# Performance work log

Hardware: AMD Instinct MI355X
Metric: run time of the kernel (lower is better)

Reference implementation:

```python
import jax, jax.numpy as jnp
import numpy as np


def _mk_mat(rows):
    # rows: list of 3 lists of (B,) arrays, written as matrix rows.
    # torch code stacks rows at dim=2, which transposes: replicate that.
    M = jnp.stack([jnp.stack(r, axis=1) for r in rows], axis=1)  # (B,3,3) written-rows
    return jnp.swapaxes(M, 1, 2)  # matches torch.stack(..., dim=2)


def _compose_mats(affine, scale, translate, shear):
    B = affine.shape[0]
    one = jnp.ones((B,), affine.dtype)
    zero = jnp.zeros((B,), affine.dtype)
    cx, sx = jnp.cos(affine[:, 0]), jnp.sin(affine[:, 0])
    cy, sy = jnp.cos(affine[:, 1]), jnp.sin(affine[:, 1])
    cz, sz = jnp.cos(affine[:, 2]), jnp.sin(affine[:, 2])
    rot_x = _mk_mat([[one, zero, zero], [zero, cx, -sx], [zero, sx, cx]])
    rot_y = _mk_mat([[cy, zero, sy], [zero, one, zero], [-sy, zero, cy]])
    rot_z = _mk_mat([[cz, -sz, zero], [sz, cz, zero], [zero, zero, one]])
    scale_m = _mk_mat([[scale[:, 0], zero, zero], [zero, scale[:, 1], zero], [zero, zero, scale[:, 2]]])
    t = jnp.tan(shear)
    shear_m = _mk_mat([[one, t[:, 0], t[:, 1]], [t[:, 2], one, t[:, 3]], [t[:, 4], t[:, 5], one]])
    trans = translate[:, :, None]  # (B,3,1)
    mat3 = shear_m @ (scale_m @ (rot_z @ (rot_y @ rot_x)))  # (B,3,3)
    inv3 = jnp.linalg.inv(mat3)
    mat = jnp.concatenate([mat3, trans], axis=-1)  # (B,3,4)
    inv_trans = jnp.matmul(-inv3, trans)
    inv_mat = jnp.concatenate([inv3, inv_trans], axis=-1)
    return mat, inv_mat


def _affine_grid(mat, D, H, W):
    # torch affine_grid, align_corners=False: coord_i = (2*i+1)/n - 1
    dt = mat.dtype
    xs = (jnp.arange(W, dtype=dt) + 0.5) * (2.0 / W) - 1.0
    ys = (jnp.arange(H, dtype=dt) + 0.5) * (2.0 / H) - 1.0
    zs = (jnp.arange(D, dtype=dt) + 0.5) * (2.0 / D) - 1.0
    zz, yy, xx = jnp.meshgrid(zs, ys, xs, indexing='ij')
    coords = jnp.stack([xx, yy, zz], axis=-1)  # (D,H,W,3) in (x,y,z) order
    grid = jnp.einsum('bkj,dhwj->bdhwk', mat[:, :, :3], coords) + mat[:, None, None, None, :, 3]
    return grid  # (B,D,H,W,3)


def _grid_sample_trilinear(src, grid):
    # torch grid_sample, mode='bilinear' (trilinear in 3D), padding zeros, align_corners=False
    B, C, D, H, W = src.shape
    ix = (grid[..., 0] + 1.0) * (W * 0.5) - 0.5
    iy = (grid[..., 1] + 1.0) * (H * 0.5) - 0.5
    iz = (grid[..., 2] + 1.0) * (D * 0.5) - 0.5
    fx, fy, fz = jnp.floor(ix), jnp.floor(iy), jnp.floor(iz)
    wx, wy, wz = ix - fx, iy - fy, iz - fz  # fractional weights
    x0, y0, z0 = fx.astype(jnp.int32), fy.astype(jnp.int32), fz.astype(jnp.int32)
    x1, y1, z1 = x0 + 1, y0 + 1, z0 + 1
    N = D * H * W
    src_flat = src.reshape(B, C, N)

    def gather(z, y, x):
        valid = (x >= 0) & (x < W) & (y >= 0) & (y < H) & (z >= 0) & (z < D)
        xi = jnp.clip(x, 0, W - 1)
        yi = jnp.clip(y, 0, H - 1)
        zi = jnp.clip(z, 0, D - 1)
        idx = ((zi * H + yi) * W + xi).reshape(B, 1, N)
        v = jnp.take_along_axis(src_flat, jnp.broadcast_to(idx, (B, C, N)), axis=2)
        return v * valid.reshape(B, 1, N).astype(src.dtype)

    def w(a):
        return a.reshape(B, 1, N)

    out = (gather(z0, y0, x0) * w((1 - wz) * (1 - wy) * (1 - wx))
           + gather(z0, y0, x1) * w((1 - wz) * (1 - wy) * wx)
           + gather(z0, y1, x0) * w((1 - wz) * wy * (1 - wx))
           + gather(z0, y1, x1) * w((1 - wz) * wy * wx)
           + gather(z1, y0, x0) * w(wz * (1 - wy) * (1 - wx))
           + gather(z1, y0, x1) * w(wz * (1 - wy) * wx)
           + gather(z1, y1, x0) * w(wz * wy * (1 - wx))
           + gather(z1, y1, x1) * w(wz * wy * wx))
    return out.reshape(B, C, D, H, W)


def setup_inputs() -> dict:
    key = jax.random.key(0)
    k1, k2, k3, k4, k5 = jax.random.split(key, 5)
    B, C, D, H, W = 2, 1, 192, 192, 192
    src = jax.random.normal(k1, (B, C, D, H, W), dtype=jnp.float32)
    affine = jax.random.uniform(k2, (B, 3), dtype=jnp.float32)
    scale = jax.random.uniform(k3, (B, 3), dtype=jnp.float32)
    translate = jax.random.uniform(k4, (B, 3), dtype=jnp.float32)
    shear = jax.random.uniform(k5, (B, 6), dtype=jnp.float32)
    return {"src": src, "affine": affine, "scale": scale, "translate": translate, "shear": shear}


def reference(src, affine, scale, translate, shear):
    B, C, D, H, W = src.shape
    mat, inv_mat = _compose_mats(affine, scale, translate, shear)
    grid = _affine_grid(mat, D, H, W)
    warped = _grid_sample_trilinear(src, grid)
    return warped, mat, inv_mat
```

## Files before the change

### kernel.cpp

```cpp
#include <hip/hip_runtime.h>
#include <math.h>

#define Bv 2
#define Dv 192
#define Hv 192
#define Wv 192
#define Nv (Dv*Hv*Wv)
#define NOUT (Bv*Nv)

#define TLZ 8
#define SWID 32
#define CAPF 16000

typedef float v2f __attribute__((ext_vector_type(2)));

__device__ __forceinline__ void mm3(const float a[3][3], const float b[3][3], float c[3][3]) {
#pragma unroll
    for (int i = 0; i < 3; ++i)
#pragma unroll
        for (int j = 0; j < 3; ++j)
            c[i][j] = a[i][0]*b[0][j] + a[i][1]*b[1][j] + a[i][2]*b[2][j];
}

__global__ void compose_mats_kernel(const float* __restrict__ affine,
                                    const float* __restrict__ scale,
                                    const float* __restrict__ translate,
                                    const float* __restrict__ shear,
                                    float* __restrict__ mats_out) {
    int b = threadIdx.x;
    if (b >= Bv) return;

    float ax = affine[b*3+0], ay = affine[b*3+1], az = affine[b*3+2];
    float cx = cosf(ax), sx = sinf(ax);
    float cy = cosf(ay), sy = sinf(ay);
    float cz = cosf(az), sz = sinf(az);

    float rx[3][3] = {{1.f,0.f,0.f},{0.f,cx,sx},{0.f,-sx,cx}};
    float ry[3][3] = {{cy,0.f,-sy},{0.f,1.f,0.f},{sy,0.f,cy}};
    float rz[3][3] = {{cz,sz,0.f},{-sz,cz,0.f},{0.f,0.f,1.f}};

    float t0 = tanf(shear[b*6+0]), t1 = tanf(shear[b*6+1]), t2 = tanf(shear[b*6+2]);
    float t3 = tanf(shear[b*6+3]), t4 = tanf(shear[b*6+4]), t5 = tanf(shear[b*6+5]);
    float sh[3][3] = {{1.f,t2,t4},{t0,1.f,t5},{t1,t3,1.f}};

    float s0 = scale[b*3+0], s1 = scale[b*3+1], s2 = scale[b*3+2];

    float m1[3][3], m2[3][3], m3s[3][3], mat3[3][3];
    mm3(ry, rx, m1);
    mm3(rz, m1, m2);
#pragma unroll
    for (int j = 0; j < 3; ++j) { m3s[0][j] = s0*m2[0][j]; m3s[1][j] = s1*m2[1][j]; m3s[2][j] = s2*m2[2][j]; }
    mm3(sh, m3s, mat3);

    float tr0 = translate[b*3+0], tr1 = translate[b*3+1], tr2 = translate[b*3+2];

    float a00 = mat3[0][0], a01 = mat3[0][1], a02 = mat3[0][2];
    float a10 = mat3[1][0], a11 = mat3[1][1], a12 = mat3[1][2];
    float a20 = mat3[2][0], a21 = mat3[2][1], a22 = mat3[2][2];
    float c00 =  (a11*a22 - a12*a21);
    float c01 = -(a10*a22 - a12*a20);
    float c02 =  (a10*a21 - a11*a20);
    float det = a00*c00 + a01*c01 + a02*c02;
    float rdet = 1.0f / det;
    float inv3[3][3];
    inv3[0][0] = c00*rdet;
    inv3[0][1] = (a02*a21 - a01*a22)*rdet;
    inv3[0][2] = (a01*a12 - a02*a11)*rdet;
    inv3[1][0] = c01*rdet;
    inv3[1][1] = (a00*a22 - a02*a20)*rdet;
    inv3[1][2] = (a02*a10 - a00*a12)*rdet;
    inv3[2][0] = c02*rdet;
    inv3[2][1] = (a01*a20 - a00*a21)*rdet;
    inv3[2][2] = (a00*a11 - a01*a10)*rdet;

    float* mo = mats_out + b*12;
#pragma unroll
    for (int i = 0; i < 3; ++i) {
        mo[i*4+0] = mat3[i][0]; mo[i*4+1] = mat3[i][1]; mo[i*4+2] = mat3[i][2];
    }
    mo[0*4+3] = tr0; mo[1*4+3] = tr1; mo[2*4+3] = tr2;

    float* io = mats_out + 24 + b*12;
#pragma unroll
    for (int i = 0; i < 3; ++i) {
        io[i*4+0] = inv3[i][0]; io[i*4+1] = inv3[i][1]; io[i*4+2] = inv3[i][2];
        io[i*4+3] = -(inv3[i][0]*tr0 + inv3[i][1]*tr1 + inv3[i][2]*tr2);
    }
}

__device__ __forceinline__ float2 ld2(const float* p) {
    float2 r;
    __builtin_memcpy(&r, p, 8);
    return r;
}

__device__ __forceinline__ void gld_lds4(const float* g, float* l) {
    __builtin_amdgcn_global_load_lds(
        (const __attribute__((address_space(1))) unsigned int*)g,
        (__attribute__((address_space(3))) unsigned int*)l, 4, 0, 0);
}

__global__ __launch_bounds__(512) void warp_kernel(const float* __restrict__ src,
                                                   const float* __restrict__ mats,
                                                   float* __restrict__ out) {
    __shared__ float stage[CAPF];

    int t   = threadIdx.x;
    int lx  = t & 15;
    int ly  = (t >> 4) & 15;
    int lzt = t >> 8;

    int W0 = blockIdx.x * 16;
    int H0 = blockIdx.y * 16;
    int zt = blockIdx.z;
    int b  = zt / (Dv/TLZ);
    int Z0 = (zt % (Dv/TLZ)) * TLZ;

    const float* M = mats + b*12;
    float m00 = M[0], m01 = M[1],  m02 = M[2],  m03 = M[3];
    float m10 = M[4], m11 = M[5],  m12 = M[6],  m13 = M[7];
    float m20 = M[8], m21 = M[9],  m22 = M[10], m23 = M[11];

    float Cx = 96.0f*(m03 - m00 - m01 - m02) + 95.5f;
    float Cy = 96.0f*(m13 - m10 - m11 - m12) + 95.5f;
    float Cz = 96.0f*(m23 - m20 - m21 - m22) + 95.5f;

    const float* sb = src + (size_t)b * Nv;

    float bcx = W0 + 8.0f, bcy = H0 + 8.0f, bcz = Z0 + 4.0f;
    float cxv = fmaf(m00, bcx, fmaf(m01, bcy, fmaf(m02, bcz, Cx)));
    float cyv = fmaf(m10, bcx, fmaf(m11, bcy, fmaf(m12, bcz, Cy)));
    float czv = fmaf(m20, bcx, fmaf(m21, bcy, fmaf(m22, bcz, Cz)));
    float hxv = 7.5f*fabsf(m00) + 7.5f*fabsf(m01) + 3.5f*fabsf(m02);
    float hyv = 7.5f*fabsf(m10) + 7.5f*fabsf(m11) + 3.5f*fabsf(m12);
    float hzv = 7.5f*fabsf(m20) + 7.5f*fabsf(m21) + 3.5f*fabsf(m22);

    int xlo = (int)floorf(cxv - hxv), xhi1 = (int)floorf(cxv + hxv) + 1;
    int ylo = (int)floorf(cyv - hyv), yhi1 = (int)floorf(cyv + hyv) + 1;
    int zlo = (int)floorf(czv - hzv), zhi1 = (int)floorf(czv + hzv) + 1;

    int bx0 = min(max(xlo, 0), Wv - SWID);
    int ey_s = min(yhi1 - ylo + 1, 64);
    int nP  = (ey_s + 1) >> 1;
    int PST = 68*nP + 4;
    int ez_need = zhi1 - zlo + 1;
    int ez_s = min(ez_need, CAPF / PST);
    int by0 = min(max(ylo, 0), Hv - 2*nP);
    int bz0 = min(max(zlo + ((ez_need - ez_s) >> 1), 0), Dv - max(ez_s, 0));

    bool uok = (xhi1 >= 0) & (xlo < Wv) & (yhi1 >= 0) & (ylo < Hv) &
               (zhi1 >= 0) & (zlo < Dv) & (ez_s >= 2) & (ey_s >= 2);
    if (!uok) ez_s = 0;

    int w = W0 + lx, h = H0 + ly;
    float fw = w + 0.5f, fh = h + 0.5f;
    float fz0 = Z0 + lzt*4 + 0.5f;

    int lane = t & 63;
    int wvu  = __builtin_amdgcn_readfirstlane(t >> 6);
    int lrow = lane >> 5;
    int col  = lane & 31;
    int srcb = (bz0*Hv + by0)*Wv + bx0 + lrow*Wv + col;
    for (int dz = wvu; dz < ez_s; dz += 8) {
        int sp = srcb + dz*(Hv*Wv);
        int lb = dz*PST;
        for (int j = 0; j < nP; ++j) {
            gld_lds4(sb + sp, &stage[lb + j*68]);
            sp += 2*Wv;
        }
    }

    float ixb = fmaf(m00, fw, fmaf(m01, fh, fmaf(m02, fz0, Cx)));
    float iyb = fmaf(m10, fw, fmaf(m11, fh, fmaf(m12, fz0, Cy)));
    float izb = fmaf(m20, fw, fmaf(m21, fh, fmaf(m22, fz0, Cz)));

    asm volatile("s_waitcnt vmcnt(0)" ::: "memory");
    __syncthreads();

    auto direct_sample = [&](float ix, float iy, float iz) -> float {
        float flx = floorf(ix), fly = floorf(iy), flz = floorf(iz);
        float wx = ix - flx, wy = iy - fly, wz = iz - flz;
        int x0 = (int)flx, y0 = (int)fly, z0 = (int)flz;
        bool all_in = ((unsigned)x0 < (unsigned)(Wv-1)) &
                      ((unsigned)y0 < (unsigned)(Hv-1)) &
                      ((unsigned)z0 < (unsigned)(Dv-1));
        if (all_in) {
            const float* p = sb + ((z0*Hv + y0)*Wv + x0);
            const float* q = p + Hv*Wv;
            float2 v00 = ld2(p);
            float2 v01 = ld2(p + Wv);
            float2 v10 = ld2(q);
            float2 v11 = ld2(q + Wv);
            float c00 = fmaf(wx, v00.y - v00.x, v00.x);
            float c01 = fmaf(wx, v01.y - v01.x, v01.x);
            float c10 = fmaf(wx, v10.y - v10.x, v10.x);
            float c11 = fmaf(wx, v11.y - v11.x, v11.x);
            float c0  = fmaf(wy, c01 - c00, c00);
            float c1  = fmaf(wy, c11 - c10, c10);
            return fmaf(wz, c1 - c0, c0);
        }
        int x1 = x0 + 1, y1 = y0 + 1, z1 = z0 + 1;
        bool all_out = (x1 < 0) | (x0 >= Wv) | (y1 < 0) | (y0 >= Hv) | (z1 < 0) | (z0 >= Dv);
        if (all_out) return 0.0f;
        auto gather = [&](int zz, int yy, int xx) -> float {
            bool valid = ((unsigned)xx < (unsigned)Wv) &
                         ((unsigned)yy < (unsigned)Hv) &
                         ((unsigned)zz < (unsigned)Dv);
            int xi = min(max(xx, 0), Wv-1);
            int yi = min(max(yy, 0), Hv-1);
            int zi = min(max(zz, 0), Dv-1);
            float val = sb[(zi*Hv + yi)*Wv + xi];
            return valid ? val : 0.0f;
        };
        float owx = 1.0f - wx, owy = 1.0f - wy, owz = 1.0f - wz;
        float a;
        a  = gather(z0, y0, x0) * (owz*owy*owx);
        a += gather(z0, y0, x1) * (owz*owy*wx);
        a += gather(z0, y1, x0) * (owz*wy*owx);
        a += gather(z0, y1, x1) * (owz*wy*wx);
        a += gather(z1, y0, x0) * (wz*owy*owx);
        a += gather(z1, y0, x1) * (wz*owy*wx);
        a += gather(z1, y1, x0) * (wz*wy*owx);
        a += gather(z1, y1, x1) * (wz*wy*wx);
        return a;
    };

    float accs[4];

#pragma unroll
    for (int zp = 0; zp < 2; ++zp) {
        float zA = (float)(2*zp), zB = (float)(2*zp + 1);
        float ixA = fmaf(m02, zA, ixb), ixB = fmaf(m02, zB, ixb);
        float iyA = fmaf(m12, zA, iyb), iyB = fmaf(m12, zB, iyb);
        float izA = fmaf(m22, zA, izb), izB = fmaf(m22, zB, izb);

        float fxA = floorf(ixA), fxB = floorf(ixB);
        float fyA = floorf(iyA), fyB = floorf(iyB);
        float fzA = floorf(izA), fzB = floorf(izB);

        int dxA = (int)fxA - bx0, dxB = (int)fxB - bx0;
        int dyA = (int)fyA - by0, dyB = (int)fyB - by0;
        int dzA = (int)fzA - bz0, dzB = (int)fzB - bz0;

        bool okA = ((unsigned)dxA <= (unsigned)(SWID-2)) &
                   ((unsigned)dyA <= (unsigned)(ey_s-2)) &
                   ((unsigned)dzA <= (unsigned)(ez_s-2));
        bool okB = ((unsigned)dxB <= (unsigned)(SWID-2)) &
                   ((unsigned)dyB <= (unsigned)(ey_s-2)) &
                   ((unsigned)dzB <= (unsigned)(ez_s-2));

        if (uok && __all(okA & okB)) {
            v2f wx2; wx2.x = ixA - fxA; wx2.y = ixB - fxB;
            v2f wy2; wy2.x = iyA - fyA; wy2.y = iyB - fyB;
            v2f wz2; wz2.x = izA - fzA; wz2.y = izB - fzB;

            int oddA = dyA & 1, oddB = dyB & 1;
            int o00A = dzA*PST + 34*dyA - (oddA << 1) + dxA;
            int o00B = dzB*PST + 34*dyB - (oddB << 1) + dxB;
            int o01A = o00A + 32 + (oddA << 2);
            int o01B = o00B + 32 + (oddB << 2);
            int o10A = o00A + PST, o10B = o00B + PST;
            int o11A = o01A + PST, o11B = o01B + PST;

            v2f v000; v000.x = stage[o00A];   v000.y = stage[o00B];
            v2f v001; v001.x = stage[o00A+1]; v001.y = stage[o00B+1];
            v2f v010; v010.x = stage[o01A];   v010.y = stage[o01B];
            v2f v011; v011.x = stage[o01A+1]; v011.y = stage[o01B+1];
            v2f v100; v100.x = stage[o10A];   v100.y = stage[o10B];
            v2f v101; v101.x = stage[o10A+1]; v101.y = stage[o10B+1];
            v2f v110; v110.x = stage[o11A];   v110.y = stage[o11B];
            v2f v111; v111.x = stage[o11A+1]; v111.y = stage[o11B+1];

            v2f c00 = wx2*(v001 - v000) + v000;
            v2f c01 = wx2*(v011 - v010) + v010;
            v2f c10 = wx2*(v101 - v100) + v100;
            v2f c11 = wx2*(v111 - v110) + v110;
            v2f c0  = wy2*(c01 - c00) + c00;
            v2f c1  = wy2*(c11 - c10) + c10;
            v2f r   = wz2*(c1 - c0) + c0;
            accs[2*zp]   = r.x;
            accs[2*zp+1] = r.y;
        } else {
            accs[2*zp]   = direct_sample(ixA, iyA, izA);
            accs[2*zp+1] = direct_sample(ixB, iyB, izB);
        }
    }

#pragma unroll
    for (int zi = 0; zi < 4; ++zi) {
        int z = Z0 + lzt*4 + zi;
        __builtin_nontemporal_store(accs[zi], &out[((size_t)(b*Dv + z)*Hv + h)*Wv + w]);
    }
}

extern "C" void kernel_launch(void* const* d_in, const int* in_sizes, int n_in,
                              void* d_out, int out_size, void* d_ws, size_t ws_size,
                              hipStream_t stream) {
    const float* src       = (const float*)d_in[0];
    const float* affine    = (const float*)d_in[1];
    const float* scale     = (const float*)d_in[2];
    const float* translate = (const float*)d_in[3];
    const float* shear     = (const float*)d_in[4];

    float* out  = (float*)d_out;
    float* mats = out + NOUT;

    compose_mats_kernel<<<1, 64, 0, stream>>>(affine, scale, translate, shear, mats);

    dim3 grid(Wv/16, Hv/16, (Dv/TLZ)*Bv);
    warp_kernel<<<grid, 512, 0, stream>>>(src, mats, out);
}
```

Baseline: 57.33 us.

## Stage source tile in LDS as truncated bf16 with register-staged loads

```diff
diff --git a/kernel.cpp b/kernel.cpp
--- a/kernel.cpp
+++ b/kernel.cpp
@@ -10,7 +10,7 @@
 
 #define TLZ 8
 #define SWID 32
-#define CAPF 16000
+#define CAPH 18432
 
 typedef float v2f __attribute__((ext_vector_type(2)));
 
@@ -94,16 +94,10 @@
     return r;
 }
 
-__device__ __forceinline__ void gld_lds4(const float* g, float* l) {
-    __builtin_amdgcn_global_load_lds(
-        (const __attribute__((address_space(1))) unsigned int*)g,
-        (__attribute__((address_space(3))) unsigned int*)l, 4, 0, 0);
-}
-
 __global__ __launch_bounds__(512) void warp_kernel(const float* __restrict__ src,
                                                    const float* __restrict__ mats,
                                                    float* __restrict__ out) {
-    __shared__ float stage[CAPF];
+    __shared__ unsigned short lsh[CAPH];
 
     int t   = threadIdx.x;
     int lx  = t & 15;
@@ -140,12 +134,13 @@
     int zlo = (int)floorf(czv - hzv), zhi1 = (int)floorf(czv + hzv) + 1;
 
     int bx0 = min(max(xlo, 0), Wv - SWID);
-    int ey_s = min(yhi1 - ylo + 1, 64);
-    int nP  = (ey_s + 1) >> 1;
-    int PST = 68*nP + 4;
+    int ey_s  = min(yhi1 - ylo + 1, 64);
+    int eyPad = (ey_s + 3) & ~3;
+    int PSTh  = eyPad*34 + 2;
+    int dpl   = PSTh >> 1;
     int ez_need = zhi1 - zlo + 1;
-    int ez_s = min(ez_need, CAPF / PST);
-    int by0 = min(max(ylo, 0), Hv - 2*nP);
+    int ez_s = min(ez_need, CAPH / PSTh);
+    int by0 = min(max(ylo, 0), Hv - eyPad);
     int bz0 = min(max(zlo + ((ez_need - ez_s) >> 1), 0), Dv - max(ez_s, 0));
 
     bool uok = (xhi1 >= 0) & (xlo < Wv) & (yhi1 >= 0) & (ylo < Hv) &
@@ -156,17 +151,23 @@
     float fw = w + 0.5f, fh = h + 0.5f;
     float fz0 = Z0 + lzt*4 + 0.5f;
 
-    int lane = t & 63;
-    int wvu  = __builtin_amdgcn_readfirstlane(t >> 6);
-    int lrow = lane >> 5;
-    int col  = lane & 31;
-    int srcb = (bz0*Hv + by0)*Wv + bx0 + lrow*Wv + col;
-    for (int dz = wvu; dz < ez_s; dz += 8) {
-        int sp = srcb + dz*(Hv*Wv);
-        int lb = dz*PST;
-        for (int j = 0; j < nP; ++j) {
-            gld_lds4(sb + sp, &stage[lb + j*68]);
-            sp += 2*Wv;
+    {
+        int lane = t & 63;
+        int wvu  = __builtin_amdgcn_readfirstlane(t >> 6);
+        int rq   = lane >> 4;
+        int cp   = lane & 15;
+        for (int dz = wvu; dz < ez_s; dz += 8) {
+            int gp = ((bz0 + dz)*Hv + by0)*Wv + bx0 + 2*cp;
+            int lp = dz*PSTh + 2*cp;
+#pragma unroll 2
+            for (int r0 = 0; r0 < eyPad; r0 += 4) {
+                int dy = min(r0 + rq, ey_s - 1);
+                float2 v = ld2(sb + gp + dy*Wv);
+                unsigned ux = __builtin_bit_cast(unsigned, v.x);
+                unsigned uy = __builtin_bit_cast(unsigned, v.y);
+                unsigned pk = (uy & 0xffff0000u) | (ux >> 16);
+                *reinterpret_cast<unsigned*>(&lsh[lp + (r0 + rq)*34]) = pk;
+            }
         }
     }
 
@@ -174,8 +175,19 @@
     float iyb = fmaf(m10, fw, fmaf(m11, fh, fmaf(m12, fz0, Cy)));
     float izb = fmaf(m20, fw, fmaf(m21, fh, fmaf(m22, fz0, Cz)));
 
-    asm volatile("s_waitcnt vmcnt(0)" ::: "memory");
     __syncthreads();
+
+    const unsigned* ls32 = reinterpret_cast<const unsigned*>(lsh);
+
+    auto tap2 = [&](int dw, int par) -> float2 {
+        unsigned w0 = ls32[dw], w1 = ls32[dw + 1];
+        unsigned al = __builtin_amdgcn_alignbit(w1, w0, 16);
+        unsigned pk = par ? al : w0;
+        float2 r;
+        r.x = __builtin_bit_cast(float, pk << 16);
+        r.y = __builtin_bit_cast(float, pk & 0xffff0000u);
+        return r;
+    };
 
     auto direct_sample = [&](float ix, float iy, float iz) -> float {
         float flx = floorf(ix), fly = floorf(iy), flz = floorf(iz);
@@ -254,22 +266,27 @@
             v2f wy2; wy2.x = iyA - fyA; wy2.y = iyB - fyB;
             v2f wz2; wz2.x = izA - fzA; wz2.y = izB - fzB;
 
-            int oddA = dyA & 1, oddB = dyB & 1;
-            int o00A = dzA*PST + 34*dyA - (oddA << 1) + dxA;
-            int o00B = dzB*PST + 34*dyB - (oddB << 1) + dxB;
-            int o01A = o00A + 32 + (oddA << 2);
-            int o01B = o00B + 32 + (oddB << 2);
-            int o10A = o00A + PST, o10B = o00B + PST;
-            int o11A = o01A + PST, o11B = o01B + PST;
-
-            v2f v000; v000.x = stage[o00A];   v000.y = stage[o00B];
-            v2f v001; v001.x = stage[o00A+1]; v001.y = stage[o00B+1];
-            v2f v010; v010.x = stage[o01A];   v010.y = stage[o01B];
-            v2f v011; v011.x = stage[o01A+1]; v011.y = stage[o01B+1];
-            v2f v100; v100.x = stage[o10A];   v100.y = stage[o10B];
-            v2f v101; v101.x = stage[o10A+1]; v101.y = stage[o10B+1];
-            v2f v110; v110.x = stage[o11A];   v110.y = stage[o11B];
-            v2f v111; v111.x = stage[o11A+1]; v111.y = stage[o11B+1];
+            int kA = dxA >> 1, pA = dxA & 1;
+            int kB = dxB >> 1, pB = dxB & 1;
+            int r00A = dzA*dpl + dyA*17 + kA;
+            int r00B = dzB*dpl + dyB*17 + kB;
+            int r01A = r00A + 17,  r01B = r00B + 17;
+            int r10A = r00A + dpl, r10B = r00B + dpl;
+            int r11A = r01A + dpl, r11B = r01B + dpl;
+
+            float2 q00A = tap2(r00A, pA), q00B = tap2(r00B, pB);
+            float2 q01A = tap2(r01A, pA), q01B = tap2(r01B, pB);
+            float2 q10A = tap2(r10A, pA), q10B = tap2(r10B, pB);
+            float2 q11A = tap2(r11A, pA), q11B = tap2(r11B, pB);
+
+            v2f v000; v000.x = q00A.x; v000.y = q00B.x;
+            v2f v001; v001.x = q00A.y; v001.y = q00B.y;
+            v2f v010; v010.x = q01A.x; v010.y = q01B.x;
+            v2f v011; v011.x = q01A.y; v011.y = q01B.y;
+            v2f v100; v100.x = q10A.x; v100.y = q10B.x;
+            v2f v101; v101.x = q10A.y; v101.y = q10B.y;
+            v2f v110; v110.x = q11A.x; v110.y = q11B.x;
+            v2f v111; v111.x = q11A.y; v111.y = q11B.y;
 
             v2f c00 = wx2*(v001 - v000) + v000;
             v2f c01 = wx2*(v011 - v010) + v010;
```

Result: faster. 50.07 us (-12.7%).
